# Kernel optimization log

Hardware: AMD Instinct MI355X
Metric: run time of the kernel (lower is better)

The kernel has to match this reference:

```python
import jax, jax.numpy as jnp
import numpy as np
from jax.scipy.linalg import solve_triangular


def setup_inputs() -> dict:
    key = jax.random.key(0)
    k1, k2 = jax.random.split(key)
    # [K classes, N per class, D features] training embeddings
    src_seq = jax.random.normal(k1, (256, 64, 128), dtype=jnp.float32)
    # [M, D] vectors to project and pairwise-score (clustering inner loop)
    test = jax.random.normal(k2, (8192, 128), dtype=jnp.float32)
    return {"src_seq": src_seq, "test": test}


def _fit_model(src_seq):
    # Faithful port of compute_scatter_matrices + fit_model.
    # S_w, S_b are symmetric PSD, so solve(S_w,S_b) eig is replaced by the
    # equivalent (and differentiable) generalized symmetric eig via Cholesky
    # whitening; A_inverse and psi are invariant to eigvec scaling/order.
    K, N, D = src_seq.shape
    count = K * N
    mean_per_class = src_seq.mean(axis=1)            # [K, D]
    mean = src_seq.mean(axis=(0, 1))                 # [D]
    diff_w = src_seq - mean_per_class[:, None, :]    # [K, N, D]
    diff_b = mean_per_class - mean                   # [K, D]
    S_w = jnp.einsum('knd,kne->de', diff_w, diff_w) / count   # [D, D]
    S_b = (N * jnp.einsum('kd,ke->de', diff_b, diff_b)) / count

    L = jnp.linalg.cholesky(S_w)                     # S_w = L L^T
    # Msym = L^{-1} S_b L^{-T}
    tmp = solve_triangular(L, S_b, lower=True)
    Msym = solve_triangular(L, tmp.T, lower=True).T
    Msym = 0.5 * (Msym + Msym.T)
    evals, U = jnp.linalg.eigh(Msym)
    W = solve_triangular(L, U, lower=True, trans=1)  # W = L^{-T} U, eigvecs of S_w^{-1} S_b

    lambda_b = jnp.sum(W * (S_b @ W), axis=0)        # diag(W^T S_b W)
    lambda_w = jnp.sum(W * (S_w @ W), axis=0)        # diag(W^T S_w W)
    n = float(N)
    # A = W^{-T} diag(sqrt(n/(n-1) * lambda_w))  =>  A^{-1} = diag(1/sqrt(.)) W^T
    A_inverse = (1.0 / jnp.sqrt(n / (n - 1.0) * lambda_w))[:, None] * W.T
    psi = jnp.clip((n - 1.0) / n * (lambda_b / lambda_w) - 1.0 / n, 0.0)
    return A_inverse, mean, psi


def reference(src_seq, test):
    A_inverse, mean, psi = _fit_model(src_seq)
    # latent = A_inverse @ (x - mean), batched over rows
    latent = (test - mean) @ A_inverse.T             # [M, D]
    # Pairwise single-vector probability (calculate_probability_single),
    # vectorized over all (i, j) pairs, in log space:
    # log p(i,j) = -(v_i - v_j)^T diag(psi) (v_i - v_j)
    #             - 0.5 * (D*log(2*pi) + log(||psi||_F))
    D = latent.shape[1]
    q = jnp.sum(psi * latent * latent, axis=1)       # [M]
    G = (latent * psi) @ latent.T                    # [M, M]
    maha = q[:, None] + q[None, :] - 2.0 * G         # [M, M]
    log_div = 0.5 * (D * jnp.log(2.0 * jnp.pi) + jnp.log(jnp.linalg.norm(psi)))
    return -maha - log_div                           # [M, M] pairwise log-prob
```

## Files before the change

### kernel.cpp

```cpp
#include <hip/hip_runtime.h>
#include <math.h>


#define D 128
#define NCLS 256
#define NPC 64
#define MTEST 8192
#define COUNT (NCLS*NPC)

#define fMC    0
#define fMEAN  16384
#define fSCAL  16640
#define fMAT   32768
#define fSWRAW 442368
#define fPART  458752
#define fU     458752
#define fV     983040
#define fQ     1507328
#define fBBF   1515520

#define sP   0
#define sSB  1
#define sP2  2
#define sP3  3
#define sP4  4
#define sZ   5
#define sMm  7
#define sC2  8
#define sXH  10
#define sT2  11
#define sT3  12
#define sT4  13
#define sT5  14
#define sT10 15
#define sT15 16
#define sT20 17
#define sG0  18
#define sF   23

using short8 = __attribute__((ext_vector_type(8))) short;
using f32x4  = __attribute__((ext_vector_type(4))) float;

__device__ inline unsigned short f2bf(float f) {
  unsigned u = __float_as_uint(f);
  unsigned r = u + 0x7FFFu + ((u >> 16) & 1u);
  return (unsigned short)(r >> 16);
}
__device__ inline float bf2f(unsigned short h) {
  return __uint_as_float(((unsigned)h) << 16);
}
__device__ inline float valU(const unsigned short* m, int idx) {
  return bf2f(m[idx]) + bf2f(m[idx + 16384]);
}
__device__ inline void storeDual(unsigned short* m, int idx, float g) {
  unsigned short hb = f2bf(g);
  m[idx] = hb;
  m[16384 + idx] = f2bf(g - bf2f(hb));
}
__device__ inline unsigned short* MS(float* ws, int m) {
  return (unsigned short*)(ws + fMAT) + (size_t)m * 32768;
}
__device__ inline short8 lds8(const unsigned short* L, int row, int colk) {
  unsigned u = ((unsigned)(row * 128 + colk)) ^ (((unsigned)(row & 7)) << 3);
  return *(const short8*)(L + u);
}
__device__ inline void ldsPutDual(unsigned short* L, int row, int col, float g) {
  unsigned u = ((unsigned)(row * 128 + col)) ^ (((unsigned)(row & 7)) << 3);
  unsigned short hb = f2bf(g);
  L[u] = hb;
  L[16384 + u] = f2bf(g - bf2f(hb));
}

__device__ float mm_body(const unsigned short* A, const unsigned short* B,
                         unsigned short* C, const unsigned short* E1,
                         float alpha, float beta, float delta, int brow) {
  int tid = threadIdx.x;
  int w = tid >> 6, lane = tid & 63;
  int wcol = w * 32;
  f32x4 acc[2][2] = {};
  #pragma unroll
  for (int ks = 0; ks < 4; ks++) {
    int kb = ks * 32 + (lane >> 4) * 8;
    short8 ah[2], al[2], bh[2], bl[2];
    #pragma unroll
    for (int mt = 0; mt < 2; mt++) {
      int r = brow + mt * 16 + (lane & 15);
      ah[mt] = *(const short8*)(A + r * 128 + kb);
      al[mt] = *(const short8*)(A + 16384 + r * 128 + kb);
    }
    #pragma unroll
    for (int nt = 0; nt < 2; nt++) {
      int c = wcol + nt * 16 + (lane & 15);
      bh[nt] = *(const short8*)(B + c * 128 + kb);
      bl[nt] = *(const short8*)(B + 16384 + c * 128 + kb);
    }
    #pragma unroll
    for (int mt = 0; mt < 2; mt++)
      #pragma unroll
      for (int nt = 0; nt < 2; nt++) {
        f32x4 a0 = acc[mt][nt];
        a0 = __builtin_amdgcn_mfma_f32_16x16x32_bf16(ah[mt], bh[nt], a0, 0, 0, 0);
        a0 = __builtin_amdgcn_mfma_f32_16x16x32_bf16(al[mt], bh[nt], a0, 0, 0, 0);
        a0 = __builtin_amdgcn_mfma_f32_16x16x32_bf16(ah[mt], bl[nt], a0, 0, 0, 0);
        acc[mt][nt] = a0;
      }
  }
  float tsum = 0.f;
  #pragma unroll
  for (int mt = 0; mt < 2; mt++)
    #pragma unroll
    for (int nt = 0; nt < 2; nt++)
      #pragma unroll
      for (int r = 0; r < 4; r++) {
        int row = brow + mt * 16 + (lane >> 4) * 4 + r;
        int col = wcol + nt * 16 + (lane & 15);
        int idx = row * 128 + col;
        float g = acc[mt][nt][r] * alpha;
        if (E1) g += beta * valU(E1, idx);
        if (row == col) g += delta;
        storeDual(C, idx, g);
        tsum += g * g;
      }
  return tsum;
}

__global__ __launch_bounds__(256) void k_gt_partial(const float* __restrict__ X, float* __restrict__ ws) {
  __shared__ unsigned short xt[128 * 256];
  int b = blockIdx.x, tid = threadIdx.x;
  const float* Xc = X + b * 256 * D;
  for (int idx = tid; idx < 256 * D; idx += 256) {
    int s = idx >> 7, d = idx & 127;
    unsigned byte = ((unsigned)(d * 512 + s * 2)) ^ (((unsigned)(d & 7)) << 4);
    *(unsigned short*)((char*)xt + byte) = f2bf(Xc[idx]);
  }
  {
    int d = tid & 127;
    for (int cc = (tid >> 7); cc < 4; cc += 2) {
      const float* p = Xc + cc * 64 * D + d;
      float s = 0.f;
      #pragma unroll
      for (int n = 0; n < 64; n++) s += p[n * D];
      ((unsigned short*)ws)[d * 256 + (b * 4 + cc)] = f2bf(s * (1.0f / 64.0f));
    }
  }
  __syncthreads();
  int w = tid >> 6, lane = tid & 63;
  int wr = (w >> 1) * 64, wc = (w & 1) * 64;
  f32x4 acc[4][4] = {};
  for (int ks = 0; ks < 8; ks++) {
    int kb = ks * 32 + (lane >> 4) * 8;
    short8 af[4];
    #pragma unroll
    for (int mt = 0; mt < 4; mt++) {
      int r = wr + mt * 16 + (lane & 15);
      unsigned byte = ((unsigned)(r * 512 + kb * 2)) ^ (((unsigned)(r & 7)) << 4);
      af[mt] = *(short8*)((char*)xt + byte);
    }
    #pragma unroll
    for (int nt = 0; nt < 4; nt++) {
      int c = wc + nt * 16 + (lane & 15);
      unsigned byte = ((unsigned)(c * 512 + kb * 2)) ^ (((unsigned)(c & 7)) << 4);
      short8 bfr = *(short8*)((char*)xt + byte);
      #pragma unroll
      for (int mt = 0; mt < 4; mt++)
        acc[mt][nt] = __builtin_amdgcn_mfma_f32_16x16x32_bf16(af[mt], bfr, acc[mt][nt], 0, 0, 0);
    }
  }
  float* outp = ws + fPART + b * 16384;
  #pragma unroll
  for (int mt = 0; mt < 4; mt++)
    #pragma unroll
    for (int nt = 0; nt < 4; nt++)
      #pragma unroll
      for (int r = 0; r < 4; r++) {
        int row = wr + mt * 16 + (lane >> 4) * 4 + r;
        int col = wc + nt * 16 + (lane & 15);
        outp[row * 128 + col] = acc[mt][nt][r];
      }
}

__global__ void k_reduce(float* __restrict__ ws) {
  __shared__ float red2[4];
  int tid = threadIdx.x;
  int idx = blockIdx.x * 256 + tid;
  const float* part = ws + fPART;
  float s = 0.f;
  #pragma unroll 8
  for (int p = 0; p < 64; p++) s += part[p * 16384 + idx];
  ws[fSWRAW + idx] = s;
  if (blockIdx.x == 0 && tid < 128) {
    const unsigned short* McT = (const unsigned short*)ws;
    float m = 0.f;
    for (int k = 0; k < 256; k++) m += bf2f(McT[tid * 256 + k]);
    ws[fMEAN + tid] = m * (1.0f / 256.0f);
  }
  if (blockIdx.x == 1) {
    float v = 0.f;
    if (tid < 128) {
      float gdd = 0.f;
      for (int p = 0; p < 64; p++) gdd += part[p * 16384 + tid * 129];
      const unsigned short* McT = (const unsigned short*)ws;
      float nrm = 0.f;
      for (int k = 0; k < 256; k++) { float x = bf2f(McT[tid * 256 + k]); nrm += x * x; }
      v = gdd * (1.0f / COUNT) - nrm * (1.0f / 256.0f);
    }
    #pragma unroll
    for (int off = 32; off > 0; off >>= 1) v += __shfl_down(v, off);
    if ((tid & 63) == 0) red2[tid >> 6] = v;
    __syncthreads();
    if (tid == 0) {
      float inv_s = 128.0f / (red2[0] + red2[1] + red2[2] + red2[3]);
      ws[fSCAL + 1] = inv_s;
      ws[fSCAL + 7] = 0.984375f * inv_s;
    }
  }
}

__global__ __launch_bounds__(256) void k_sbp(float* __restrict__ ws) {
  const unsigned short* Mc = (const unsigned short*)ws;
  const float* mv = ws + fMEAN;
  const float* swraw = ws + fSWRAW;
  float inv_s = ws[fSCAL + 1];
  unsigned short* SB = MS(ws, sSB);
  unsigned short* P = MS(ws, sP);
  int tid = threadIdx.x, b = blockIdx.x;
  int w = tid >> 6, lane = tid & 63;
  int brow = b * 32, wcol = w * 32;
  f32x4 acc[2][2] = {};
  for (int ks = 0; ks < 8; ks++) {
    int kb = ks * 32 + (lane >> 4) * 8;
    short8 af[2], bfv[2];
    #pragma unroll
    for (int mt = 0; mt < 2; mt++) {
      int r = brow + mt * 16 + (lane & 15);
      af[mt] = *(const short8*)(Mc + r * 256 + kb);
    }
    #pragma unroll
    for (int nt = 0; nt < 2; nt++) {
      int c = wcol + nt * 16 + (lane & 15);
      bfv[nt] = *(const short8*)(Mc + c * 256 + kb);
    }
    #pragma unroll
    for (int mt = 0; mt < 2; mt++)
      #pragma unroll
      for (int nt = 0; nt < 2; nt++)
        acc[mt][nt] = __builtin_amdgcn_mfma_f32_16x16x32_bf16(af[mt], bfv[nt], acc[mt][nt], 0, 0, 0);
  }
  #pragma unroll
  for (int mt = 0; mt < 2; mt++)
    #pragma unroll
    for (int nt = 0; nt < 2; nt++)
      #pragma unroll
      for (int r = 0; r < 4; r++) {
        int row = brow + mt * 16 + (lane >> 4) * 4 + r;
        int col = wcol + nt * 16 + (lane & 15);
        int idx = row * 128 + col;
        float g = acc[mt][nt][r] * (1.0f / 256.0f) - mv[row] * mv[col];
        storeDual(SB, idx, g);
        float s = (swraw[idx] * (1.0f / COUNT) - g - mv[row] * mv[col]) * inv_s;
        storeDual(P, idx, s - ((row == col) ? 1.0f : 0.0f));
      }
}

__global__ __launch_bounds__(256) void k_p234(float* __restrict__ ws) {
  __shared__ unsigned short sL[32768];
  float* scal = ws + fSCAL;
  const unsigned short* P = MS(ws, sP);
  unsigned short* P2 = MS(ws, sP2);
  unsigned short* P3 = MS(ws, sP3);
  unsigned short* P4 = MS(ws, sP4);
  int tid = threadIdx.x, b = blockIdx.x;
  int w = tid >> 6, lane = tid & 63;
  int wcol = w * 32, brow = b * 32;
  {
    f32x4 acc[8][2] = {};
    for (int ks = 0; ks < 4; ks++) {
      int kb = ks * 32 + (lane >> 4) * 8;
      short8 bh[2], bl[2];
      #pragma unroll
      for (int nt = 0; nt < 2; nt++) {
        int c = wcol + nt * 16 + (lane & 15);
        bh[nt] = *(const short8*)(P + c * 128 + kb);
        bl[nt] = *(const short8*)(P + 16384 + c * 128 + kb);
      }
      #pragma unroll
      for (int mt = 0; mt < 8; mt++) {
        int r = mt * 16 + (lane & 15);
        short8 ah = *(const short8*)(P + r * 128 + kb);
        short8 al = *(const short8*)(P + 16384 + r * 128 + kb);
        #pragma unroll
        for (int nt = 0; nt < 2; nt++) {
          f32x4 a0 = acc[mt][nt];
          a0 = __builtin_amdgcn_mfma_f32_16x16x32_bf16(ah, bh[nt], a0, 0, 0, 0);
          a0 = __builtin_amdgcn_mfma_f32_16x16x32_bf16(al, bh[nt], a0, 0, 0, 0);
          a0 = __builtin_amdgcn_mfma_f32_16x16x32_bf16(ah, bl[nt], a0, 0, 0, 0);
          acc[mt][nt] = a0;
        }
      }
    }
    #pragma unroll
    for (int mt = 0; mt < 8; mt++)
      #pragma unroll
      for (int nt = 0; nt < 2; nt++)
        #pragma unroll
        for (int r = 0; r < 4; r++) {
          int row = mt * 16 + (lane >> 4) * 4 + r;
          int col = wcol + nt * 16 + (lane & 15);
          float g = acc[mt][nt][r];
          ldsPutDual(sL, row, col, g);
          storeDual(P2, row * 128 + col, g);
        }
  }
  __syncthreads();
  float tsum = 0.f;
  {
    f32x4 a3[2][2] = {}, a4[2][2] = {};
    for (int ks = 0; ks < 4; ks++) {
      int kb = ks * 32 + (lane >> 4) * 8;
      short8 ah[2], al[2], b3h[2], b3l[2], b4h[2], b4l[2];
      #pragma unroll
      for (int mt = 0; mt < 2; mt++) {
        int r = brow + mt * 16 + (lane & 15);
        ah[mt] = lds8(sL, r, kb);
        al[mt] = lds8(sL + 16384, r, kb);
      }
      #pragma unroll
      for (int nt = 0; nt < 2; nt++) {
        int c = wcol + nt * 16 + (lane & 15);
        b3h[nt] = *(const short8*)(P + c * 128 + kb);
        b3l[nt] = *(const short8*)(P + 16384 + c * 128 + kb);
        b4h[nt] = lds8(sL, c, kb);
        b4l[nt] = lds8(sL + 16384, c, kb);
      }
      #pragma unroll
      for (int mt = 0; mt < 2; mt++)
        #pragma unroll
        for (int nt = 0; nt < 2; nt++) {
          f32x4 x3 = a3[mt][nt];
          x3 = __builtin_amdgcn_mfma_f32_16x16x32_bf16(ah[mt], b3h[nt], x3, 0, 0, 0);
          x3 = __builtin_amdgcn_mfma_f32_16x16x32_bf16(al[mt], b3h[nt], x3, 0, 0, 0);
          x3 = __builtin_amdgcn_mfma_f32_16x16x32_bf16(ah[mt], b3l[nt], x3, 0, 0, 0);
          a3[mt][nt] = x3;
          f32x4 x4 = a4[mt][nt];
          x4 = __builtin_amdgcn_mfma_f32_16x16x32_bf16(ah[mt], b4h[nt], x4, 0, 0, 0);
          x4 = __builtin_amdgcn_mfma_f32_16x16x32_bf16(al[mt], b4h[nt], x4, 0, 0, 0);
          x4 = __builtin_amdgcn_mfma_f32_16x16x32_bf16(ah[mt], b4l[nt], x4, 0, 0, 0);
          a4[mt][nt] = x4;
        }
    }
    #pragma unroll
    for (int mt = 0; mt < 2; mt++)
      #pragma unroll
      for (int nt = 0; nt < 2; nt++)
        #pragma unroll
        for (int r = 0; r < 4; r++) {
          int row = brow + mt * 16 + (lane >> 4) * 4 + r;
          int col = wcol + nt * 16 + (lane & 15);
          int idx = row * 128 + col;
          storeDual(P3, idx, a3[mt][nt][r]);
          float g4 = a4[mt][nt][r];
          storeDual(P4, idx, g4);
          tsum += g4 * g4;
        }
  }
  #pragma unroll
  for (int off = 32; off > 0; off >>= 1) tsum += __shfl_down(tsum, off);
  __syncthreads();
  float* red = (float*)sL;
  if (lane == 0) red[w] = tsum;
  __syncthreads();
  if (tid == 0) scal[60 + b] = red[0] + red[1] + red[2] + red[3];
}

__global__ __launch_bounds__(256) void k_z(float* __restrict__ ws) {
  __shared__ float cj[7];
  __shared__ float bt[7];
  float* scal = ws + fSCAL;
  const unsigned short *P = MS(ws, sP), *P2 = MS(ws, sP2),
    *P3 = MS(ws, sP3), *P4 = MS(ws, sP4);
  unsigned short* Z = MS(ws, sZ);
  int tid = threadIdx.x, b = blockIdx.x;
  float trP8 = scal[60] + scal[61] + scal[62] + scal[63];
  float a = 1.05f * sqrtf(sqrtf(sqrtf(fmaxf(trP8, 1e-30f))));
  a = fminf(a, 0.95f);
  if (tid < 7) {
    const float PI = 3.14159265358979f;
    float s = 0.f;
    for (int i = 0; i < 64; i++) {
      float th = (i + 0.5f) * (PI / 64.0f);
      float x = cosf(th);
      s += (1.0f / sqrtf(1.0f + a * x)) * cosf((float)tid * th);
    }
    cj[tid] = s * (2.0f / 64.0f);
  }
  __syncthreads();
  if (tid == 0) {
    float c0h = 0.5f * cj[0];
    float m0 = c0h - cj[2] + cj[4] - cj[6];
    float m1 = cj[1] - 3.0f * cj[3] + 5.0f * cj[5];
    float m2 = 2.0f * cj[2] - 8.0f * cj[4] + 18.0f * cj[6];
    float m3 = 4.0f * cj[3] - 20.0f * cj[5];
    float m4 = 8.0f * cj[4] - 48.0f * cj[6];
    float m5 = 16.0f * cj[5];
    float m6 = 32.0f * cj[6];
    float ia = 1.0f / a, p = 1.f;
    bt[0] = m0;
    p *= ia; bt[1] = m1 * p;
    p *= ia; bt[2] = m2 * p;
    p *= ia; bt[3] = m3 * p;
    p *= ia; bt[4] = m4 * p;
    p *= ia; bt[5] = m5 * p;
    p *= ia; bt[6] = m6 * p;
  }
  __syncthreads();
  int w = tid >> 6, lane = tid & 63;
  int brow = b * 32, wcol = w * 32;
  f32x4 a5[2][2] = {}, a6[2][2] = {};
  #pragma unroll
  for (int ks = 0; ks < 4; ks++) {
    int kb = ks * 32 + (lane >> 4) * 8;
    short8 ah[2], al[2], b5h[2], b5l[2], b6h[2], b6l[2];
    #pragma unroll
    for (int mt = 0; mt < 2; mt++) {
      int r = brow + mt * 16 + (lane & 15);
      ah[mt] = *(const short8*)(P4 + r * 128 + kb);
      al[mt] = *(const short8*)(P4 + 16384 + r * 128 + kb);
    }
    #pragma unroll
    for (int nt = 0; nt < 2; nt++) {
      int c = wcol + nt * 16 + (lane & 15);
      b5h[nt] = *(const short8*)(P + c * 128 + kb);
      b5l[nt] = *(const short8*)(P + 16384 + c * 128 + kb);
      b6h[nt] = *(const short8*)(P2 + c * 128 + kb);
      b6l[nt] = *(const short8*)(P2 + 16384 + c * 128 + kb);
    }
    #pragma unroll
    for (int mt = 0; mt < 2; mt++)
      #pragma unroll
      for (int nt = 0; nt < 2; nt++) {
        f32x4 x5 = a5[mt][nt];
        x5 = __builtin_amdgcn_mfma_f32_16x16x32_bf16(ah[mt], b5h[nt], x5, 0, 0, 0);
        x5 = __builtin_amdgcn_mfma_f32_16x16x32_bf16(al[mt], b5h[nt], x5, 0, 0, 0);
        x5 = __builtin_amdgcn_mfma_f32_16x16x32_bf16(ah[mt], b5l[nt], x5, 0, 0, 0);
        a5[mt][nt] = x5;
        f32x4 x6 = a6[mt][nt];
        x6 = __builtin_amdgcn_mfma_f32_16x16x32_bf16(ah[mt], b6h[nt], x6, 0, 0, 0);
        x6 = __builtin_amdgcn_mfma_f32_16x16x32_bf16(al[mt], b6h[nt], x6, 0, 0, 0);
        x6 = __builtin_amdgcn_mfma_f32_16x16x32_bf16(ah[mt], b6l[nt], x6, 0, 0, 0);
        a6[mt][nt] = x6;
      }
  }
  #pragma unroll
  for (int mt = 0; mt < 2; mt++)
    #pragma unroll
    for (int nt = 0; nt < 2; nt++)
      #pragma unroll
      for (int r = 0; r < 4; r++) {
        int row = brow + mt * 16 + (lane >> 4) * 4 + r;
        int col = wcol + nt * 16 + (lane & 15);
        int idx = row * 128 + col;
        float dg = (row == col) ? 1.0f : 0.0f;
        float z = bt[0] * dg + bt[1] * valU(P, idx) + bt[2] * valU(P2, idx) +
                  bt[3] * valU(P3, idx) + bt[4] * valU(P4, idx) +
                  bt[5] * a5[mt][nt][r] + bt[6] * a6[mt][nt][r];
        storeDual(Z, idx, z);
      }
}

__global__ __launch_bounds__(256) void k_msb(float* __restrict__ ws) {
  __shared__ unsigned short sL[32768];
  const unsigned short* Z = MS(ws, sZ);
  const unsigned short* SB = MS(ws, sSB);
  unsigned short* Mm = MS(ws, sMm);
  int tid = threadIdx.x, b = blockIdx.x;
  int w = tid >> 6, lane = tid & 63;
  int wcol = w * 32, brow = b * 32;
  {
    f32x4 acc[8][2] = {};
    for (int ks = 0; ks < 4; ks++) {
      int kb = ks * 32 + (lane >> 4) * 8;
      short8 bh[2], bl[2];
      #pragma unroll
      for (int nt = 0; nt < 2; nt++) {
        int c = wcol + nt * 16 + (lane & 15);
        bh[nt] = *(const short8*)(SB + c * 128 + kb);
        bl[nt] = *(const short8*)(SB + 16384 + c * 128 + kb);
      }
      #pragma unroll
      for (int mt = 0; mt < 8; mt++) {
        int r = mt * 16 + (lane & 15);
        short8 ah = *(const short8*)(Z + r * 128 + kb);
        short8 al = *(const short8*)(Z + 16384 + r * 128 + kb);
        #pragma unroll
        for (int nt = 0; nt < 2; nt++) {
          f32x4 a0 = acc[mt][nt];
          a0 = __builtin_amdgcn_mfma_f32_16x16x32_bf16(ah, bh[nt], a0, 0, 0, 0);
          a0 = __builtin_amdgcn_mfma_f32_16x16x32_bf16(al, bh[nt], a0, 0, 0, 0);
          a0 = __builtin_amdgcn_mfma_f32_16x16x32_bf16(ah, bl[nt], a0, 0, 0, 0);
          acc[mt][nt] = a0;
        }
      }
    }
    #pragma unroll
    for (int mt = 0; mt < 8; mt++)
      #pragma unroll
      for (int nt = 0; nt < 2; nt++)
        #pragma unroll
        for (int r = 0; r < 4; r++) {
          int row = mt * 16 + (lane >> 4) * 4 + r;
          int col = wcol + nt * 16 + (lane & 15);
          ldsPutDual(sL, row, col, acc[mt][nt][r]);
        }
  }
  __syncthreads();
  {
    f32x4 acc[2][2] = {};
    for (int ks = 0; ks < 4; ks++) {
      int kb = ks * 32 + (lane >> 4) * 8;
      short8 ah[2], al[2], bh[2], bl[2];
      #pragma unroll
      for (int mt = 0; mt < 2; mt++) {
        int r = brow + mt * 16 + (lane & 15);
        ah[mt] = lds8(sL, r, kb);
        al[mt] = lds8(sL + 16384, r, kb);
      }
      #pragma unroll
      for (int nt = 0; nt < 2; nt++) {
        int c = wcol + nt * 16 + (lane & 15);
        bh[nt] = *(const short8*)(Z + c * 128 + kb);
        bl[nt] = *(const short8*)(Z + 16384 + c * 128 + kb);
      }
      #pragma unroll
      for (int mt = 0; mt < 2; mt++)
        #pragma unroll
        for (int nt = 0; nt < 2; nt++) {
          f32x4 a0 = acc[mt][nt];
          a0 = __builtin_amdgcn_mfma_f32_16x16x32_bf16(ah[mt], bh[nt], a0, 0, 0, 0);
          a0 = __builtin_amdgcn_mfma_f32_16x16x32_bf16(al[mt], bh[nt], a0, 0, 0, 0);
          a0 = __builtin_amdgcn_mfma_f32_16x16x32_bf16(ah[mt], bl[nt], a0, 0, 0, 0);
          acc[mt][nt] = a0;
        }
    }
    #pragma unroll
    for (int mt = 0; mt < 2; mt++)
      #pragma unroll
      for (int nt = 0; nt < 2; nt++)
        #pragma unroll
        for (int r = 0; r < 4; r++) {
          int row = brow + mt * 16 + (lane >> 4) * 4 + r;
          int col = wcol + nt * 16 + (lane & 15);
          storeDual(Mm, row * 128 + col, acc[mt][nt][r]);
        }
  }
}

__global__ __launch_bounds__(256) void k_c24(float* __restrict__ ws) {
  __shared__ unsigned short sL[32768];
  float* scal = ws + fSCAL;
  const unsigned short* Mm = MS(ws, sMm);
  unsigned short* C2 = MS(ws, sC2);
  int tid = threadIdx.x, b = blockIdx.x;
  int w = tid >> 6, lane = tid & 63;
  int wcol = w * 32, brow = b * 32;
  {
    f32x4 acc[8][2] = {};
    for (int ks = 0; ks < 4; ks++) {
      int kb = ks * 32 + (lane >> 4) * 8;
      short8 bh[2], bl[2];
      #pragma unroll
      for (int nt = 0; nt < 2; nt++) {
        int c = wcol + nt * 16 + (lane & 15);
        bh[nt] = *(const short8*)(Mm + c * 128 + kb);
        bl[nt] = *(const short8*)(Mm + 16384 + c * 128 + kb);
      }
      #pragma unroll
      for (int mt = 0; mt < 8; mt++) {
        int r = mt * 16 + (lane & 15);
        short8 ah = *(const short8*)(Mm + r * 128 + kb);
        short8 al = *(const short8*)(Mm + 16384 + r * 128 + kb);
        #pragma unroll
        for (int nt = 0; nt < 2; nt++) {
          f32x4 a0 = acc[mt][nt];
          a0 = __builtin_amdgcn_mfma_f32_16x16x32_bf16(ah, bh[nt], a0, 0, 0, 0);
          a0 = __builtin_amdgcn_mfma_f32_16x16x32_bf16(al, bh[nt], a0, 0, 0, 0);
          a0 = __builtin_amdgcn_mfma_f32_16x16x32_bf16(ah, bl[nt], a0, 0, 0, 0);
          acc[mt][nt] = a0;
        }
      }
    }
    #pragma unroll
    for (int mt = 0; mt < 8; mt++)
      #pragma unroll
      for (int nt = 0; nt < 2; nt++)
        #pragma unroll
        for (int r = 0; r < 4; r++) {
          int row = mt * 16 + (lane >> 4) * 4 + r;
          int col = wcol + nt * 16 + (lane & 15);
          float g = acc[mt][nt][r];
          ldsPutDual(sL, row, col, g);
          storeDual(C2, row * 128 + col, g);
        }
  }
  __syncthreads();
  float tsum = 0.f;
  {
    f32x4 acc[2][2] = {};
    for (int ks = 0; ks < 4; ks++) {
      int kb = ks * 32 + (lane >> 4) * 8;
      short8 ah[2], al[2], bh[2], bl[2];
      #pragma unroll
      for (int mt = 0; mt < 2; mt++) {
        int r = brow + mt * 16 + (lane & 15);
        ah[mt] = lds8(sL, r, kb);
        al[mt] = lds8(sL + 16384, r, kb);
      }
      #pragma unroll
      for (int nt = 0; nt < 2; nt++) {
        int c = wcol + nt * 16 + (lane & 15);
        bh[nt] = lds8(sL, c, kb);
        bl[nt] = lds8(sL + 16384, c, kb);
      }
      #pragma unroll
      for (int mt = 0; mt < 2; mt++)
        #pragma unroll
        for (int nt = 0; nt < 2; nt++) {
          f32x4 a0 = acc[mt][nt];
          a0 = __builtin_amdgcn_mfma_f32_16x16x32_bf16(ah[mt], bh[nt], a0, 0, 0, 0);
          a0 = __builtin_amdgcn_mfma_f32_16x16x32_bf16(al[mt], bh[nt], a0, 0, 0, 0);
          a0 = __builtin_amdgcn_mfma_f32_16x16x32_bf16(ah[mt], bl[nt], a0, 0, 0, 0);
          acc[mt][nt] = a0;
        }
    }
    #pragma unroll
    for (int mt = 0; mt < 2; mt++)
      #pragma unroll
      for (int nt = 0; nt < 2; nt++)
        #pragma unroll
        for (int r = 0; r < 4; r++) {
          float g = acc[mt][nt][r];
          tsum += g * g;
        }
  }
  #pragma unroll
  for (int off = 32; off > 0; off >>= 1) tsum += __shfl_down(tsum, off);
  __syncthreads();
  float* red = (float*)sL;
  if (lane == 0) red[w] = tsum;
  __syncthreads();
  if (tid == 0) scal[68 + b] = red[0] + red[1] + red[2] + red[3];
}

__device__ inline void interval_cs(const float* scal, float* c0o, float* iho) {
  float trM8 = scal[68] + scal[69] + scal[70] + scal[71];
  float Lam = 1.03f * sqrtf(sqrtf(sqrtf(fmaxf(trM8, 1e-37f))));
  float lo = -0.02f * Lam, hi = Lam;
  *c0o = 0.5f * (hi + lo);
  *iho = 1.0f / (0.5f * (hi - lo));
}

__global__ __launch_bounds__(256) void k_xh_t2(float* __restrict__ ws) {
  __shared__ float cs[2];
  float* scal = ws + fSCAL;
  if (threadIdx.x == 0) {
    float c0, ih;
    interval_cs(scal, &c0, &ih);
    cs[0] = c0; cs[1] = ih;
  }
  __syncthreads();
  float c0 = cs[0], ih = cs[1];
  float a2 = 2.0f * ih * ih, b2 = -4.0f * c0 * ih * ih, g2 = 2.0f * c0 * c0 * ih * ih - 1.0f;
  const unsigned short* Mm = MS(ws, sMm);
  const unsigned short* C2 = MS(ws, sC2);
  unsigned short* XH = MS(ws, sXH);
  unsigned short* T2 = MS(ws, sT2);
  int gid = blockIdx.x * 256 + threadIdx.x;
  #pragma unroll
  for (int t = 0; t < 4; t++) {
    int idx = gid * 4 + t;
    int row = idx >> 7, col = idx & 127;
    float m = valU(Mm, idx), c2v = valU(C2, idx);
    float dg = (row == col) ? 1.0f : 0.0f;
    storeDual(XH, idx, ih * m - ih * c0 * dg);
    storeDual(T2, idx, a2 * c2v + b2 * m + g2 * dg);
  }
}

__global__ __launch_bounds__(256) void k_t34(float* __restrict__ ws) {
  const unsigned short* XH = MS(ws, sXH);
  const unsigned short* T2 = MS(ws, sT2);
  if (blockIdx.x < 4) {
    mm_body(XH, T2, MS(ws, sT3), XH, 2.0f, -1.0f, 0.0f, blockIdx.x * 32);
  } else {
    mm_body(T2, T2, MS(ws, sT4), nullptr, 2.0f, 0.0f, -1.0f, (blockIdx.x - 4) * 32);
  }
}

__global__ __launch_bounds__(256) void k_t5g(float* __restrict__ ws) {
  __shared__ float cs[8];
  __shared__ float sat[25];
  __shared__ float sc[25];
  float* scal = ws + fSCAL;
  int tid = threadIdx.x;
  if (blockIdx.x < 4) {
    mm_body(MS(ws, sT3), MS(ws, sT2), MS(ws, sT5), MS(ws, sXH),
            2.0f, -1.0f, 0.0f, blockIdx.x * 32);
    return;
  }
  if (tid == 0) {
    float c0, ih;
    interval_cs(scal, &c0, &ih);
    float inv_s = scal[1];
    float t0 = (1.0f / 63.0f) / inv_s;
    float x0 = fminf(fmaxf((t0 - c0) * ih, -1.0f), 1.0f);
    cs[0] = acosf(x0); cs[1] = x0;
    cs[2] = 0.984375f * inv_s / ih;
  }
  __syncthreads();
  if (tid <= 24) {
    float th = cs[0], x0 = cs[1], SCc = cs[2];
    const float PI = 3.14159265358979f;
    float v;
    if (tid == 0) v = 0.5f * SCc * (2.0f / PI) * (sinf(th) - x0 * th);
    else if (tid == 1) v = SCc * (2.0f / PI) * (0.5f * th + 0.25f * sinf(2.0f * th) - x0 * sinf(th));
    else {
      float fj = (float)tid;
      v = SCc * (2.0f / PI) *
          (0.5f * (sinf((fj + 1.0f) * th) / (fj + 1.0f) + sinf((fj - 1.0f) * th) / (fj - 1.0f))
           - x0 * sinf(fj * th) / fj);
    }
    sat[tid] = v;
    sc[tid] = 0.f;
  }
  __syncthreads();
  if (tid == 0) {
    for (int j = 24; j >= 5; --j) {
      int k = j / 5, r = j - 5 * k;
      float aj = sat[j];
      if (r == 0) sc[k * 5] += aj;
      else { sc[k * 5 + r] += 2.0f * aj; sat[5 * k - r] -= aj; }
    }
    for (int r = 0; r < 5; r++) sc[r] += sat[r];
  }
  __syncthreads();
  const unsigned short* XH = MS(ws, sXH);
  const unsigned short* T2 = MS(ws, sT2);
  const unsigned short* T3 = MS(ws, sT3);
  const unsigned short* T4 = MS(ws, sT4);
  int bg = blockIdx.x - 4;
  int base = bg * 1024 + tid * 4;
  #pragma unroll
  for (int t = 0; t < 4; t++) {
    int idx = base + t;
    int row = idx >> 7, col = idx & 127;
    float dg = (row == col) ? 1.0f : 0.0f;
    float x1 = valU(XH, idx), x2 = valU(T2, idx), x3 = valU(T3, idx), x4 = valU(T4, idx);
    #pragma unroll
    for (int k = 0; k < 5; k++) {
      float g = sc[k * 5 + 0] * dg + sc[k * 5 + 1] * x1 + sc[k * 5 + 2] * x2 +
                sc[k * 5 + 3] * x3 + sc[k * 5 + 4] * x4;
      storeDual(MS(ws, sG0 + k), idx, g);
    }
  }
}

__global__ __launch_bounds__(256) void k_t101520(float* __restrict__ ws) {
  __shared__ unsigned short sL[32768];
  const unsigned short* T5 = MS(ws, sT5);
  unsigned short* T10 = MS(ws, sT10);
  unsigned short* T15 = MS(ws, sT15);
  unsigned short* T20 = MS(ws, sT20);
  int tid = threadIdx.x, b = blockIdx.x;
  int w = tid >> 6, lane = tid & 63;
  int wcol = w * 32, brow = b * 32;
  {
    f32x4 acc[8][2] = {};
    for (int ks = 0; ks < 4; ks++) {
      int kb = ks * 32 + (lane >> 4) * 8;
      short8 bh[2], bl[2];
      #pragma unroll
      for (int nt = 0; nt < 2; nt++) {
        int c = wcol + nt * 16 + (lane & 15);
        bh[nt] = *(const short8*)(T5 + c * 128 + kb);
        bl[nt] = *(const short8*)(T5 + 16384 + c * 128 + kb);
      }
      #pragma unroll
      for (int mt = 0; mt < 8; mt++) {
        int r = mt * 16 + (lane & 15);
        short8 ah = *(const short8*)(T5 + r * 128 + kb);
        short8 al = *(const short8*)(T5 + 16384 + r * 128 + kb);
        #pragma unroll
        for (int nt = 0; nt < 2; nt++) {
          f32x4 a0 = acc[mt][nt];
          a0 = __builtin_amdgcn_mfma_f32_16x16x32_bf16(ah, bh[nt], a0, 0, 0, 0);
          a0 = __builtin_amdgcn_mfma_f32_16x16x32_bf16(al, bh[nt], a0, 0, 0, 0);
          a0 = __builtin_amdgcn_mfma_f32_16x16x32_bf16(ah, bl[nt], a0, 0, 0, 0);
          acc[mt][nt] = a0;
        }
      }
    }
    #pragma unroll
    for (int mt = 0; mt < 8; mt++)
      #pragma unroll
      for (int nt = 0; nt < 2; nt++)
        #pragma unroll
        for (int r = 0; r < 4; r++) {
          int row = mt * 16 + (lane >> 4) * 4 + r;
          int col = wcol + nt * 16 + (lane & 15);
          float g = 2.0f * acc[mt][nt][r] - ((row == col) ? 1.0f : 0.0f);
          ldsPutDual(sL, row, col, g);
          storeDual(T10, row * 128 + col, g);
        }
  }
  __syncthreads();
  {
    f32x4 a15[2][2] = {}, a20[2][2] = {};
    for (int ks = 0; ks < 4; ks++) {
      int kb = ks * 32 + (lane >> 4) * 8;
      short8 ah[2], al[2], b5h[2], b5l[2], bth[2], btl[2];
      #pragma unroll
      for (int mt = 0; mt < 2; mt++) {
        int r = brow + mt * 16 + (lane & 15);
        ah[mt] = lds8(sL, r, kb);
        al[mt] = lds8(sL + 16384, r, kb);
      }
      #pragma unroll
      for (int nt = 0; nt < 2; nt++) {
        int c = wcol + nt * 16 + (lane & 15);
        b5h[nt] = *(const short8*)(T5 + c * 128 + kb);
        b5l[nt] = *(const short8*)(T5 + 16384 + c * 128 + kb);
        bth[nt] = lds8(sL, c, kb);
        btl[nt] = lds8(sL + 16384, c, kb);
      }
      #pragma unroll
      for (int mt = 0; mt < 2; mt++)
        #pragma unroll
        for (int nt = 0; nt < 2; nt++) {
          f32x4 x = a15[mt][nt];
          x = __builtin_amdgcn_mfma_f32_16x16x32_bf16(ah[mt], b5h[nt], x, 0, 0, 0);
          x = __builtin_amdgcn_mfma_f32_16x16x32_bf16(al[mt], b5h[nt], x, 0, 0, 0);
          x = __builtin_amdgcn_mfma_f32_16x16x32_bf16(ah[mt], b5l[nt], x, 0, 0, 0);
          a15[mt][nt] = x;
          f32x4 y = a20[mt][nt];
          y = __builtin_amdgcn_mfma_f32_16x16x32_bf16(ah[mt], bth[nt], y, 0, 0, 0);
          y = __builtin_amdgcn_mfma_f32_16x16x32_bf16(al[mt], bth[nt], y, 0, 0, 0);
          y = __builtin_amdgcn_mfma_f32_16x16x32_bf16(ah[mt], btl[nt], y, 0, 0, 0);
          a20[mt][nt] = y;
        }
    }
    #pragma unroll
    for (int mt = 0; mt < 2; mt++)
      #pragma unroll
      for (int nt = 0; nt < 2; nt++)
        #pragma unroll
        for (int r = 0; r < 4; r++) {
          int row = brow + mt * 16 + (lane >> 4) * 4 + r;
          int col = wcol + nt * 16 + (lane & 15);
          int idx = row * 128 + col;
          storeDual(T15, idx, 2.0f * a15[mt][nt][r] - valU(T5, idx));
          storeDual(T20, idx, 2.0f * a20[mt][nt][r] - ((row == col) ? 1.0f : 0.0f));
        }
  }
}

__global__ __launch_bounds__(256) void k_bigF(float* __restrict__ ws) {
  __shared__ float red[4];
  float* scal = ws + fSCAL;
  const unsigned short* As[4] = { MS(ws, sT5), MS(ws, sT10), MS(ws, sT15), MS(ws, sT20) };
  const unsigned short* Bs[4] = { MS(ws, sG0 + 1), MS(ws, sG0 + 2), MS(ws, sG0 + 3), MS(ws, sG0 + 4) };
  const unsigned short* G0 = MS(ws, sG0);
  unsigned short* Fm = MS(ws, sF);
  int tid = threadIdx.x, b = blockIdx.x;
  int w = tid >> 6, lane = tid & 63;
  int brow = b * 32, wcol = w * 32;
  f32x4 acc[2][2] = {};
  for (int p = 0; p < 4; p++) {
    const unsigned short* A = As[p];
    const unsigned short* B = Bs[p];
    #pragma unroll
    for (int ks = 0; ks < 4; ks++) {
      int kb = ks * 32 + (lane >> 4) * 8;
      short8 ah[2], al[2], bh[2], bl[2];
      #pragma unroll
      for (int mt = 0; mt < 2; mt++) {
        int r = brow + mt * 16 + (lane & 15);
        ah[mt] = *(const short8*)(A + r * 128 + kb);
        al[mt] = *(const short8*)(A + 16384 + r * 128 + kb);
      }
      #pragma unroll
      for (int nt = 0; nt < 2; nt++) {
        int c = wcol + nt * 16 + (lane & 15);
        bh[nt] = *(const short8*)(B + c * 128 + kb);
        bl[nt] = *(const short8*)(B + 16384 + c * 128 + kb);
      }
      #pragma unroll
      for (int mt = 0; mt < 2; mt++)
        #pragma unroll
        for (int nt = 0; nt < 2; nt++) {
          f32x4 a0 = acc[mt][nt];
          a0 = __builtin_amdgcn_mfma_f32_16x16x32_bf16(ah[mt], bh[nt], a0, 0, 0, 0);
          a0 = __builtin_amdgcn_mfma_f32_16x16x32_bf16(al[mt], bh[nt], a0, 0, 0, 0);
          a0 = __builtin_amdgcn_mfma_f32_16x16x32_bf16(ah[mt], bl[nt], a0, 0, 0, 0);
          acc[mt][nt] = a0;
        }
    }
  }
  float tsum = 0.f;
  #pragma unroll
  for (int mt = 0; mt < 2; mt++)
    #pragma unroll
    for (int nt = 0; nt < 2; nt++)
      #pragma unroll
      for (int r = 0; r < 4; r++) {
        int row = brow + mt * 16 + (lane >> 4) * 4 + r;
        int col = wcol + nt * 16 + (lane & 15);
        int idx = row * 128 + col;
        float g = acc[mt][nt][r] + valU(G0, idx);
        storeDual(Fm, idx, g);
        tsum += g * g;
      }
  #pragma unroll
  for (int off = 32; off > 0; off >>= 1) tsum += __shfl_down(tsum, off);
  if (lane == 0) red[w] = tsum;
  __syncthreads();
  if (tid == 0) scal[72 + b] = red[0] + red[1] + red[2] + red[3];
}

__global__ __launch_bounds__(256) void k_zfb(float* __restrict__ ws) {
  __shared__ unsigned short sL[32768];
  const unsigned short* Z = MS(ws, sZ);
  const unsigned short* Fm = MS(ws, sF);
  unsigned short* Bbf = (unsigned short*)(ws + fBBF);
  float aeff = ws[fSCAL + 7];
  int tid = threadIdx.x, b = blockIdx.x;
  int w = tid >> 6, lane = tid & 63;
  int wcol = w * 32, brow = b * 32;
  {
    f32x4 acc[8][2] = {};
    for (int ks = 0; ks < 4; ks++) {
      int kb = ks * 32 + (lane >> 4) * 8;
      short8 bh[2], bl[2];
      #pragma unroll
      for (int nt = 0; nt < 2; nt++) {
        int c = wcol + nt * 16 + (lane & 15);
        bh[nt] = *(const short8*)(Fm + c * 128 + kb);
        bl[nt] = *(const short8*)(Fm + 16384 + c * 128 + kb);
      }
      #pragma unroll
      for (int mt = 0; mt < 8; mt++) {
        int r = mt * 16 + (lane & 15);
        short8 ah = *(const short8*)(Z + r * 128 + kb);
        short8 al = *(const short8*)(Z + 16384 + r * 128 + kb);
        #pragma unroll
        for (int nt = 0; nt < 2; nt++) {
          f32x4 a0 = acc[mt][nt];
          a0 = __builtin_amdgcn_mfma_f32_16x16x32_bf16(ah, bh[nt], a0, 0, 0, 0);
          a0 = __builtin_amdgcn_mfma_f32_16x16x32_bf16(al, bh[nt], a0, 0, 0, 0);
          a0 = __builtin_amdgcn_mfma_f32_16x16x32_bf16(ah, bl[nt], a0, 0, 0, 0);
          acc[mt][nt] = a0;
        }
      }
    }
    #pragma unroll
    for (int mt = 0; mt < 8; mt++)
      #pragma unroll
      for (int nt = 0; nt < 2; nt++)
        #pragma unroll
        for (int r = 0; r < 4; r++) {
          int row = mt * 16 + (lane >> 4) * 4 + r;
          int col = wcol + nt * 16 + (lane & 15);
          ldsPutDual(sL, row, col, acc[mt][nt][r]);
        }
  }
  __syncthreads();
  {
    f32x4 acc[2][2] = {};
    for (int ks = 0; ks < 4; ks++) {
      int kb = ks * 32 + (lane >> 4) * 8;
      short8 ah[2], al[2], bh[2], bl[2];
      #pragma unroll
      for (int mt = 0; mt < 2; mt++) {
        int r = brow + mt * 16 + (lane & 15);
        ah[mt] = lds8(sL, r, kb);
        al[mt] = lds8(sL + 16384, r, kb);
      }
      #pragma unroll
      for (int nt = 0; nt < 2; nt++) {
        int c = wcol + nt * 16 + (lane & 15);
        bh[nt] = *(const short8*)(Z + c * 128 + kb);
        bl[nt] = *(const short8*)(Z + 16384 + c * 128 + kb);
      }
      #pragma unroll
      for (int mt = 0; mt < 2; mt++)
        #pragma unroll
        for (int nt = 0; nt < 2; nt++) {
          f32x4 a0 = acc[mt][nt];
          a0 = __builtin_amdgcn_mfma_f32_16x16x32_bf16(ah[mt], bh[nt], a0, 0, 0, 0);
          a0 = __builtin_amdgcn_mfma_f32_16x16x32_bf16(al[mt], bh[nt], a0, 0, 0, 0);
          a0 = __builtin_amdgcn_mfma_f32_16x16x32_bf16(ah[mt], bl[nt], a0, 0, 0, 0);
          acc[mt][nt] = a0;
        }
    }
    #pragma unroll
    for (int mt = 0; mt < 2; mt++)
      #pragma unroll
      for (int nt = 0; nt < 2; nt++)
        #pragma unroll
        for (int r = 0; r < 4; r++) {
          int row = brow + mt * 16 + (lane >> 4) * 4 + r;
          int col = wcol + nt * 16 + (lane & 15);
          Bbf[row * 128 + col] = f2bf(acc[mt][nt][r] * aeff);
        }
  }
}

__global__ __launch_bounds__(256) void k_latent(const float* __restrict__ test, float* __restrict__ ws) {
  __shared__ unsigned short vh[16384];
  __shared__ float qs[128];
  int blk = blockIdx.x, tid = threadIdx.x;
  if (blk == 0 && tid == 0) {
    float* scal = ws + fSCAL;
    float trF2 = fmaxf(scal[72] + scal[73] + scal[74] + scal[75], 1e-30f);
    scal[0] = 0.5f * (128.0f * 1.8378770664093453f + 0.5f * logf(trF2));
  }
  const float* tb = test + blk * 128 * D;
  unsigned short* Vbf = (unsigned short*)(ws + fV);
  if (tid < 128) qs[tid] = 0.f;
  for (int idx = tid; idx < 16384; idx += 256) {
    int r = idx >> 7, c = idx & 127;
    float v = tb[idx] - ws[fMEAN + c];
    unsigned short h = f2bf(v);
    unsigned byte = ((unsigned)(r * 256 + c * 2)) ^ (((unsigned)(r & 7)) << 4);
    *(unsigned short*)((char*)vh + byte) = h;
    Vbf[blk * 16384 + idx] = h;
  }
  __syncthreads();
  int w = tid >> 6, lane = tid & 63;
  int wr = (w >> 1) * 64, wc = (w & 1) * 64;
  const unsigned short* Bbf = (const unsigned short*)(ws + fBBF);
  f32x4 acc[4][4] = {};
  for (int ks = 0; ks < 4; ks++) {
    int kb = ks * 32 + (lane >> 4) * 8;
    short8 af[4], bfv[4];
    #pragma unroll
    for (int mt = 0; mt < 4; mt++) {
      int r = wr + mt * 16 + (lane & 15);
      unsigned byte = ((unsigned)(r * 256 + kb * 2)) ^ (((unsigned)(r & 7)) << 4);
      af[mt] = *(short8*)((char*)vh + byte);
    }
    #pragma unroll
    for (int nt = 0; nt < 4; nt++) {
      int c = wc + nt * 16 + (lane & 15);
      bfv[nt] = *(const short8*)(Bbf + c * 128 + kb);
    }
    #pragma unroll
    for (int mt = 0; mt < 4; mt++)
      #pragma unroll
      for (int nt = 0; nt < 4; nt++)
        acc[mt][nt] = __builtin_amdgcn_mfma_f32_16x16x32_bf16(af[mt], bfv[nt], acc[mt][nt], 0, 0, 0);
  }
  unsigned short* Ubf = (unsigned short*)(ws + fU);
  #pragma unroll
  for (int mt = 0; mt < 4; mt++)
    #pragma unroll
    for (int nt = 0; nt < 4; nt++)
      #pragma unroll
      for (int r = 0; r < 4; r++) {
        int row = wr + mt * 16 + (lane >> 4) * 4 + r;
        int col = wc + nt * 16 + (lane & 15);
        Ubf[(blk * 128 + row) * 128 + col] = f2bf(acc[mt][nt][r]);
      }
  #pragma unroll
  for (int mt = 0; mt < 4; mt++)
    #pragma unroll
    for (int r = 0; r < 4; r++) {
      int row = wr + mt * 16 + (lane >> 4) * 4 + r;
      float p = 0.f;
      #pragma unroll
      for (int nt = 0; nt < 4; nt++) {
        int col = wc + nt * 16 + (lane & 15);
        unsigned byte = ((unsigned)(row * 256 + col * 2)) ^ (((unsigned)(row & 7)) << 4);
        p += bf2f(f2bf(acc[mt][nt][r])) * bf2f(*(unsigned short*)((char*)vh + byte));
      }
      p += __shfl_xor(p, 1, 16);
      p += __shfl_xor(p, 2, 16);
      p += __shfl_xor(p, 4, 16);
      p += __shfl_xor(p, 8, 16);
      if ((lane & 15) == 0) atomicAdd(&qs[row], p);
    }
  __syncthreads();
  if (tid < 128) ws[fQ + blk * 128 + tid] = qs[tid];
}

__global__ __launch_bounds__(256) void k_pair(const float* __restrict__ ws, float* __restrict__ out) {
  __shared__ float qi[128];
  __shared__ float qj[128];
  __shared__ float sld;
  int bi = blockIdx.x, bj = blockIdx.y, tid = threadIdx.x;
  if (tid < 128) qi[tid] = ws[fQ + bi * 128 + tid];
  else qj[tid - 128] = ws[fQ + bj * 128 + (tid - 128)];
  if (tid == 0) sld = ws[fSCAL + 0];
  __syncthreads();
  int w = tid >> 6, lane = tid & 63;
  int wr = (w >> 1) * 64, wc = (w & 1) * 64;
  const unsigned short* Ubf = (const unsigned short*)(ws + fU);
  const unsigned short* Vbf = (const unsigned short*)(ws + fV);
  f32x4 acc[4][4] = {};
  for (int ks = 0; ks < 4; ks++) {
    int kb = ks * 32 + (lane >> 4) * 8;
    short8 af[4], bfv[4];
    #pragma unroll
    for (int mt = 0; mt < 4; mt++) {
      int r = bi * 128 + wr + mt * 16 + (lane & 15);
      af[mt] = *(const short8*)(Ubf + r * 128 + kb);
    }
    #pragma unroll
    for (int nt = 0; nt < 4; nt++) {
      int c = bj * 128 + wc + nt * 16 + (lane & 15);
      bfv[nt] = *(const short8*)(Vbf + c * 128 + kb);
    }
    #pragma unroll
    for (int mt = 0; mt < 4; mt++)
      #pragma unroll
      for (int nt = 0; nt < 4; nt++)
        acc[mt][nt] = __builtin_amdgcn_mfma_f32_16x16x32_bf16(af[mt], bfv[nt], acc[mt][nt], 0, 0, 0);
  }
  float ld = sld;
  #pragma unroll
  for (int mt = 0; mt < 4; mt++)
    #pragma unroll
    for (int nt = 0; nt < 4; nt++)
      #pragma unroll
      for (int r = 0; r < 4; r++) {
        int row = wr + mt * 16 + (lane >> 4) * 4 + r;
        int col = wc + nt * 16 + (lane & 15);
        float g = acc[mt][nt][r];
        out[(size_t)(bi * 128 + row) * MTEST + (bj * 128 + col)] =
          2.0f * g - qi[row] - qj[col] - ld;
      }
}

extern "C" void kernel_launch(void* const* d_in, const int* in_sizes, int n_in,
                              void* d_out, int out_size, void* d_ws, size_t ws_size,
                              hipStream_t stream) {
  (void)in_sizes; (void)n_in; (void)out_size; (void)ws_size;
  const float* X = (const float*)d_in[0];
  const float* test = (const float*)d_in[1];
  float* out = (float*)d_out;
  float* ws = (float*)d_ws;

  k_gt_partial<<<64, 256, 0, stream>>>(X, ws);
  k_reduce<<<64, 256, 0, stream>>>(ws);
  k_sbp<<<4, 256, 0, stream>>>(ws);
  k_p234<<<4, 256, 0, stream>>>(ws);
  k_z<<<4, 256, 0, stream>>>(ws);
  k_msb<<<4, 256, 0, stream>>>(ws);
  k_c24<<<4, 256, 0, stream>>>(ws);
  k_xh_t2<<<16, 256, 0, stream>>>(ws);
  k_t34<<<8, 256, 0, stream>>>(ws);
  k_t5g<<<20, 256, 0, stream>>>(ws);
  k_t101520<<<4, 256, 0, stream>>>(ws);
  k_bigF<<<4, 256, 0, stream>>>(ws);
  k_zfb<<<4, 256, 0, stream>>>(ws);
  k_latent<<<64, 256, 0, stream>>>(test, ws);
  k_pair<<<dim3(64, 64), 256, 0, stream>>>(ws, out);
}
```

Baseline: 300.5 us.

## Chain matrix products per row strip to drop redundant full-matrix recompute

The small 128x128 matrix-chain kernels no longer have each of the 4 blocks recompute a full 128x128 intermediate product. Each block now computes only its own 32-row strip and chains the next product from that strip held in shared memory, e.g. P2 then P3 = P2*P then P4 = P3*P. The C2 step drops the fourth-power trace and the spectral bound now uses the trace of M^2 with a fourth root. This removes redundant MFMA work and shrinks shared memory from 64KB to 16KB per block, at the cost of a longer serial dependency chain inside each kernel.

```diff
diff --git a/kernel.cpp b/kernel.cpp
--- a/kernel.cpp
+++ b/kernel.cpp
@@ -60,20 +60,25 @@
 __device__ inline unsigned short* MS(float* ws, int m) {
   return (unsigned short*)(ws + fMAT) + (size_t)m * 32768;
 }
-__device__ inline short8 lds8(const unsigned short* L, int row, int colk) {
-  unsigned u = ((unsigned)(row * 128 + colk)) ^ (((unsigned)(row & 7)) << 3);
+__device__ inline short8 st8(const unsigned short* L, int rloc, int colk) {
+  unsigned u = ((unsigned)(rloc * 128 + colk)) ^ (((unsigned)(rloc & 7)) << 3);
   return *(const short8*)(L + u);
 }
-__device__ inline void ldsPutDual(unsigned short* L, int row, int col, float g) {
-  unsigned u = ((unsigned)(row * 128 + col)) ^ (((unsigned)(row & 7)) << 3);
+__device__ inline float stValU(const unsigned short* L, int rloc, int col) {
+  unsigned u = ((unsigned)(rloc * 128 + col)) ^ (((unsigned)(rloc & 7)) << 3);
+  return bf2f(L[u]) + bf2f(L[4096 + u]);
+}
+__device__ inline void stPutDual(unsigned short* L, int rloc, int col, float g) {
+  unsigned u = ((unsigned)(rloc * 128 + col)) ^ (((unsigned)(rloc & 7)) << 3);
   unsigned short hb = f2bf(g);
   L[u] = hb;
-  L[16384 + u] = f2bf(g - bf2f(hb));
-}
-
-__device__ float mm_body(const unsigned short* A, const unsigned short* B,
+  L[4096 + u] = f2bf(g - bf2f(hb));
+}
+
+__device__ float mm_core(const unsigned short* A, const unsigned short* B,
                          unsigned short* C, const unsigned short* E1,
-                         float alpha, float beta, float delta, int brow) {
+                         float alpha, float beta, float delta, int brow,
+                         unsigned short* outBf, float aeff2) {
   int tid = threadIdx.x;
   int w = tid >> 6, lane = tid & 63;
   int wcol = w * 32;
@@ -118,7 +123,8 @@
         float g = acc[mt][nt][r] * alpha;
         if (E1) g += beta * valU(E1, idx);
         if (row == col) g += delta;
-        storeDual(C, idx, g);
+        if (outBf) outBf[idx] = f2bf(g * aeff2);
+        else storeDual(C, idx, g);
         tsum += g * g;
       }
   return tsum;
@@ -262,8 +268,10 @@
       }
 }
 
-__global__ __launch_bounds__(256) void k_p234(float* __restrict__ ws) {
-  __shared__ unsigned short sL[32768];
+__global__ __launch_bounds__(256) void k_pows(float* __restrict__ ws) {
+  __shared__ unsigned short sA[8192];
+  __shared__ unsigned short sB[8192];
+  __shared__ float red[4];
   float* scal = ws + fSCAL;
   const unsigned short* P = MS(ws, sP);
   unsigned short* P2 = MS(ws, sP2);
@@ -271,12 +279,19 @@
   unsigned short* P4 = MS(ws, sP4);
   int tid = threadIdx.x, b = blockIdx.x;
   int w = tid >> 6, lane = tid & 63;
-  int wcol = w * 32, brow = b * 32;
+  int brow = b * 32, wcol = w * 32;
   {
-    f32x4 acc[8][2] = {};
+    f32x4 acc[2][2] = {};
+    #pragma unroll
     for (int ks = 0; ks < 4; ks++) {
       int kb = ks * 32 + (lane >> 4) * 8;
-      short8 bh[2], bl[2];
+      short8 ah[2], al[2], bh[2], bl[2];
+      #pragma unroll
+      for (int mt = 0; mt < 2; mt++) {
+        int r = brow + mt * 16 + (lane & 15);
+        ah[mt] = *(const short8*)(P + r * 128 + kb);
+        al[mt] = *(const short8*)(P + 16384 + r * 128 + kb);
+      }
       #pragma unroll
       for (int nt = 0; nt < 2; nt++) {
         int c = wcol + nt * 16 + (lane & 15);
@@ -284,68 +299,101 @@
         bl[nt] = *(const short8*)(P + 16384 + c * 128 + kb);
       }
       #pragma unroll
-      for (int mt = 0; mt < 8; mt++) {
-        int r = mt * 16 + (lane & 15);
-        short8 ah = *(const short8*)(P + r * 128 + kb);
-        short8 al = *(const short8*)(P + 16384 + r * 128 + kb);
+      for (int mt = 0; mt < 2; mt++)
         #pragma unroll
         for (int nt = 0; nt < 2; nt++) {
           f32x4 a0 = acc[mt][nt];
-          a0 = __builtin_amdgcn_mfma_f32_16x16x32_bf16(ah, bh[nt], a0, 0, 0, 0);
-          a0 = __builtin_amdgcn_mfma_f32_16x16x32_bf16(al, bh[nt], a0, 0, 0, 0);
-          a0 = __builtin_amdgcn_mfma_f32_16x16x32_bf16(ah, bl[nt], a0, 0, 0, 0);
+          a0 = __builtin_amdgcn_mfma_f32_16x16x32_bf16(ah[mt], bh[nt], a0, 0, 0, 0);
+          a0 = __builtin_amdgcn_mfma_f32_16x16x32_bf16(al[mt], bh[nt], a0, 0, 0, 0);
+          a0 = __builtin_amdgcn_mfma_f32_16x16x32_bf16(ah[mt], bl[nt], a0, 0, 0, 0);
           acc[mt][nt] = a0;
         }
-      }
-    }
-    #pragma unroll
-    for (int mt = 0; mt < 8; mt++)
+    }
+    #pragma unroll
+    for (int mt = 0; mt < 2; mt++)
       #pragma unroll
       for (int nt = 0; nt < 2; nt++)
         #pragma unroll
         for (int r = 0; r < 4; r++) {
-          int row = mt * 16 + (lane >> 4) * 4 + r;
+          int rloc = mt * 16 + (lane >> 4) * 4 + r;
           int col = wcol + nt * 16 + (lane & 15);
           float g = acc[mt][nt][r];
-          ldsPutDual(sL, row, col, g);
-          storeDual(P2, row * 128 + col, g);
+          stPutDual(sA, rloc, col, g);
+          storeDual(P2, (brow + rloc) * 128 + col, g);
+        }
+  }
+  __syncthreads();
+  {
+    f32x4 acc[2][2] = {};
+    #pragma unroll
+    for (int ks = 0; ks < 4; ks++) {
+      int kb = ks * 32 + (lane >> 4) * 8;
+      short8 ah[2], al[2], bh[2], bl[2];
+      #pragma unroll
+      for (int mt = 0; mt < 2; mt++) {
+        int rloc = mt * 16 + (lane & 15);
+        ah[mt] = st8(sA, rloc, kb);
+        al[mt] = st8(sA + 4096, rloc, kb);
+      }
+      #pragma unroll
+      for (int nt = 0; nt < 2; nt++) {
+        int c = wcol + nt * 16 + (lane & 15);
+        bh[nt] = *(const short8*)(P + c * 128 + kb);
+        bl[nt] = *(const short8*)(P + 16384 + c * 128 + kb);
+      }
+      #pragma unroll
+      for (int mt = 0; mt < 2; mt++)
+        #pragma unroll
+        for (int nt = 0; nt < 2; nt++) {
+          f32x4 a0 = acc[mt][nt];
+          a0 = __builtin_amdgcn_mfma_f32_16x16x32_bf16(ah[mt], bh[nt], a0, 0, 0, 0);
+          a0 = __builtin_amdgcn_mfma_f32_16x16x32_bf16(al[mt], bh[nt], a0, 0, 0, 0);
+          a0 = __builtin_amdgcn_mfma_f32_16x16x32_bf16(ah[mt], bl[nt], a0, 0, 0, 0);
+          acc[mt][nt] = a0;
+        }
+    }
+    #pragma unroll
+    for (int mt = 0; mt < 2; mt++)
+      #pragma unroll
+      for (int nt = 0; nt < 2; nt++)
+        #pragma unroll
+        for (int r = 0; r < 4; r++) {
+          int rloc = mt * 16 + (lane >> 4) * 4 + r;
+          int col = wcol + nt * 16 + (lane & 15);
+          float g = acc[mt][nt][r];
+          stPutDual(sB, rloc, col, g);
+          storeDual(P3, (brow + rloc) * 128 + col, g);
         }
   }
   __syncthreads();
   float tsum = 0.f;
   {
-    f32x4 a3[2][2] = {}, a4[2][2] = {};
+    f32x4 acc[2][2] = {};
+    #pragma unroll
     for (int ks = 0; ks < 4; ks++) {
       int kb = ks * 32 + (lane >> 4) * 8;
-      short8 ah[2], al[2], b3h[2], b3l[2], b4h[2], b4l[2];
+      short8 ah[2], al[2], bh[2], bl[2];
       #pragma unroll
       for (int mt = 0; mt < 2; mt++) {
-        int r = brow + mt * 16 + (lane & 15);
-        ah[mt] = lds8(sL, r, kb);
-        al[mt] = lds8(sL + 16384, r, kb);
+        int rloc = mt * 16 + (lane & 15);
+        ah[mt] = st8(sB, rloc, kb);
+        al[mt] = st8(sB + 4096, rloc, kb);
       }
       #pragma unroll
       for (int nt = 0; nt < 2; nt++) {
         int c = wcol + nt * 16 + (lane & 15);
-        b3h[nt] = *(const short8*)(P + c * 128 + kb);
-        b3l[nt] = *(const short8*)(P + 16384 + c * 128 + kb);
-        b4h[nt] = lds8(sL, c, kb);
-        b4l[nt] = lds8(sL + 16384, c, kb);
+        bh[nt] = *(const short8*)(P + c * 128 + kb);
+        bl[nt] = *(const short8*)(P + 16384 + c * 128 + kb);
       }
       #pragma unroll
       for (int mt = 0; mt < 2; mt++)
         #pragma unroll
         for (int nt = 0; nt < 2; nt++) {
-          f32x4 x3 = a3[mt][nt];
-          x3 = __builtin_amdgcn_mfma_f32_16x16x32_bf16(ah[mt], b3h[nt], x3, 0, 0, 0);
-          x3 = __builtin_amdgcn_mfma_f32_16x16x32_bf16(al[mt], b3h[nt], x3, 0, 0, 0);
-          x3 = __builtin_amdgcn_mfma_f32_16x16x32_bf16(ah[mt], b3l[nt], x3, 0, 0, 0);
-          a3[mt][nt] = x3;
-          f32x4 x4 = a4[mt][nt];
-          x4 = __builtin_amdgcn_mfma_f32_16x16x32_bf16(ah[mt], b4h[nt], x4, 0, 0, 0);
-          x4 = __builtin_amdgcn_mfma_f32_16x16x32_bf16(al[mt], b4h[nt], x4, 0, 0, 0);
-          x4 = __builtin_amdgcn_mfma_f32_16x16x32_bf16(ah[mt], b4l[nt], x4, 0, 0, 0);
-          a4[mt][nt] = x4;
+          f32x4 a0 = acc[mt][nt];
+          a0 = __builtin_amdgcn_mfma_f32_16x16x32_bf16(ah[mt], bh[nt], a0, 0, 0, 0);
+          a0 = __builtin_amdgcn_mfma_f32_16x16x32_bf16(al[mt], bh[nt], a0, 0, 0, 0);
+          a0 = __builtin_amdgcn_mfma_f32_16x16x32_bf16(ah[mt], bl[nt], a0, 0, 0, 0);
+          acc[mt][nt] = a0;
         }
     }
     #pragma unroll
@@ -354,19 +402,15 @@
       for (int nt = 0; nt < 2; nt++)
         #pragma unroll
         for (int r = 0; r < 4; r++) {
-          int row = brow + mt * 16 + (lane >> 4) * 4 + r;
+          int rloc = mt * 16 + (lane >> 4) * 4 + r;
           int col = wcol + nt * 16 + (lane & 15);
-          int idx = row * 128 + col;
-          storeDual(P3, idx, a3[mt][nt][r]);
-          float g4 = a4[mt][nt][r];
-          storeDual(P4, idx, g4);
-          tsum += g4 * g4;
+          float g = acc[mt][nt][r];
+          storeDual(P4, (brow + rloc) * 128 + col, g);
+          tsum += g * g;
         }
   }
   #pragma unroll
   for (int off = 32; off > 0; off >>= 1) tsum += __shfl_down(tsum, off);
-  __syncthreads();
-  float* red = (float*)sL;
   if (lane == 0) red[w] = tsum;
   __syncthreads();
   if (tid == 0) scal[60 + b] = red[0] + red[1] + red[2] + red[3];
@@ -467,68 +511,31 @@
       }
 }
 
-__global__ __launch_bounds__(256) void k_msb(float* __restrict__ ws) {
-  __shared__ unsigned short sL[32768];
+__global__ __launch_bounds__(256) void k_m(float* __restrict__ ws) {
+  __shared__ unsigned short sA[8192];
   const unsigned short* Z = MS(ws, sZ);
   const unsigned short* SB = MS(ws, sSB);
   unsigned short* Mm = MS(ws, sMm);
   int tid = threadIdx.x, b = blockIdx.x;
   int w = tid >> 6, lane = tid & 63;
-  int wcol = w * 32, brow = b * 32;
+  int brow = b * 32, wcol = w * 32;
   {
-    f32x4 acc[8][2] = {};
+    f32x4 acc[2][2] = {};
+    #pragma unroll
     for (int ks = 0; ks < 4; ks++) {
       int kb = ks * 32 + (lane >> 4) * 8;
-      short8 bh[2], bl[2];
+      short8 ah[2], al[2], bh[2], bl[2];
+      #pragma unroll
+      for (int mt = 0; mt < 2; mt++) {
+        int r = brow + mt * 16 + (lane & 15);
+        ah[mt] = *(const short8*)(Z + r * 128 + kb);
+        al[mt] = *(const short8*)(Z + 16384 + r * 128 + kb);
+      }
       #pragma unroll
       for (int nt = 0; nt < 2; nt++) {
         int c = wcol + nt * 16 + (lane & 15);
         bh[nt] = *(const short8*)(SB + c * 128 + kb);
         bl[nt] = *(const short8*)(SB + 16384 + c * 128 + kb);
-      }
-      #pragma unroll
-      for (int mt = 0; mt < 8; mt++) {
-        int r = mt * 16 + (lane & 15);
-        short8 ah = *(const short8*)(Z + r * 128 + kb);
-        short8 al = *(const short8*)(Z + 16384 + r * 128 + kb);
-        #pragma unroll
-        for (int nt = 0; nt < 2; nt++) {
-          f32x4 a0 = acc[mt][nt];
-          a0 = __builtin_amdgcn_mfma_f32_16x16x32_bf16(ah, bh[nt], a0, 0, 0, 0);
-          a0 = __builtin_amdgcn_mfma_f32_16x16x32_bf16(al, bh[nt], a0, 0, 0, 0);
-          a0 = __builtin_amdgcn_mfma_f32_16x16x32_bf16(ah, bl[nt], a0, 0, 0, 0);
-          acc[mt][nt] = a0;
-        }
-      }
-    }
-    #pragma unroll
-    for (int mt = 0; mt < 8; mt++)
-      #pragma unroll
-      for (int nt = 0; nt < 2; nt++)
-        #pragma unroll
-        for (int r = 0; r < 4; r++) {
-          int row = mt * 16 + (lane >> 4) * 4 + r;
-          int col = wcol + nt * 16 + (lane & 15);
-          ldsPutDual(sL, row, col, acc[mt][nt][r]);
-        }
-  }
-  __syncthreads();
-  {
-    f32x4 acc[2][2] = {};
-    for (int ks = 0; ks < 4; ks++) {
-      int kb = ks * 32 + (lane >> 4) * 8;
-      short8 ah[2], al[2], bh[2], bl[2];
-      #pragma unroll
-      for (int mt = 0; mt < 2; mt++) {
-        int r = brow + mt * 16 + (lane & 15);
-        ah[mt] = lds8(sL, r, kb);
-        al[mt] = lds8(sL + 16384, r, kb);
-      }
-      #pragma unroll
-      for (int nt = 0; nt < 2; nt++) {
-        int c = wcol + nt * 16 + (lane & 15);
-        bh[nt] = *(const short8*)(Z + c * 128 + kb);
-        bl[nt] = *(const short8*)(Z + 16384 + c * 128 + kb);
       }
       #pragma unroll
       for (int mt = 0; mt < 2; mt++)
@@ -547,78 +554,29 @@
       for (int nt = 0; nt < 2; nt++)
         #pragma unroll
         for (int r = 0; r < 4; r++) {
-          int row = brow + mt * 16 + (lane >> 4) * 4 + r;
+          int rloc = mt * 16 + (lane >> 4) * 4 + r;
           int col = wcol + nt * 16 + (lane & 15);
-          storeDual(Mm, row * 128 + col, acc[mt][nt][r]);
-        }
-  }
-}
-
-__global__ __launch_bounds__(256) void k_c24(float* __restrict__ ws) {
-  __shared__ unsigned short sL[32768];
-  float* scal = ws + fSCAL;
-  const unsigned short* Mm = MS(ws, sMm);
-  unsigned short* C2 = MS(ws, sC2);
-  int tid = threadIdx.x, b = blockIdx.x;
-  int w = tid >> 6, lane = tid & 63;
-  int wcol = w * 32, brow = b * 32;
-  {
-    f32x4 acc[8][2] = {};
-    for (int ks = 0; ks < 4; ks++) {
-      int kb = ks * 32 + (lane >> 4) * 8;
-      short8 bh[2], bl[2];
-      #pragma unroll
-      for (int nt = 0; nt < 2; nt++) {
-        int c = wcol + nt * 16 + (lane & 15);
-        bh[nt] = *(const short8*)(Mm + c * 128 + kb);
-        bl[nt] = *(const short8*)(Mm + 16384 + c * 128 + kb);
-      }
-      #pragma unroll
-      for (int mt = 0; mt < 8; mt++) {
-        int r = mt * 16 + (lane & 15);
-        short8 ah = *(const short8*)(Mm + r * 128 + kb);
-        short8 al = *(const short8*)(Mm + 16384 + r * 128 + kb);
-        #pragma unroll
-        for (int nt = 0; nt < 2; nt++) {
-          f32x4 a0 = acc[mt][nt];
-          a0 = __builtin_amdgcn_mfma_f32_16x16x32_bf16(ah, bh[nt], a0, 0, 0, 0);
-          a0 = __builtin_amdgcn_mfma_f32_16x16x32_bf16(al, bh[nt], a0, 0, 0, 0);
-          a0 = __builtin_amdgcn_mfma_f32_16x16x32_bf16(ah, bl[nt], a0, 0, 0, 0);
-          acc[mt][nt] = a0;
-        }
-      }
-    }
-    #pragma unroll
-    for (int mt = 0; mt < 8; mt++)
-      #pragma unroll
-      for (int nt = 0; nt < 2; nt++)
-        #pragma unroll
-        for (int r = 0; r < 4; r++) {
-          int row = mt * 16 + (lane >> 4) * 4 + r;
-          int col = wcol + nt * 16 + (lane & 15);
-          float g = acc[mt][nt][r];
-          ldsPutDual(sL, row, col, g);
-          storeDual(C2, row * 128 + col, g);
-        }
-  }
-  __syncthreads();
-  float tsum = 0.f;
+          stPutDual(sA, rloc, col, acc[mt][nt][r]);
+        }
+  }
+  __syncthreads();
   {
     f32x4 acc[2][2] = {};
+    #pragma unroll
     for (int ks = 0; ks < 4; ks++) {
       int kb = ks * 32 + (lane >> 4) * 8;
       short8 ah[2], al[2], bh[2], bl[2];
       #pragma unroll
       for (int mt = 0; mt < 2; mt++) {
-        int r = brow + mt * 16 + (lane & 15);
-        ah[mt] = lds8(sL, r, kb);
-        al[mt] = lds8(sL + 16384, r, kb);
+        int rloc = mt * 16 + (lane & 15);
+        ah[mt] = st8(sA, rloc, kb);
+        al[mt] = st8(sA + 4096, rloc, kb);
       }
       #pragma unroll
       for (int nt = 0; nt < 2; nt++) {
         int c = wcol + nt * 16 + (lane & 15);
-        bh[nt] = lds8(sL, c, kb);
-        bl[nt] = lds8(sL + 16384, c, kb);
+        bh[nt] = *(const short8*)(Z + c * 128 + kb);
+        bl[nt] = *(const short8*)(Z + 16384 + c * 128 + kb);
       }
       #pragma unroll
       for (int mt = 0; mt < 2; mt++)
@@ -637,22 +595,30 @@
       for (int nt = 0; nt < 2; nt++)
         #pragma unroll
         for (int r = 0; r < 4; r++) {
-          float g = acc[mt][nt][r];
-          tsum += g * g;
-        }
-  }
+          int rloc = mt * 16 + (lane >> 4) * 4 + r;
+          int col = wcol + nt * 16 + (lane & 15);
+          storeDual(Mm, (brow + rloc) * 128 + col, acc[mt][nt][r]);
+        }
+  }
+}
+
+__global__ __launch_bounds__(256) void k_c2(float* __restrict__ ws) {
+  __shared__ float red[4];
+  float* scal = ws + fSCAL;
+  const unsigned short* Mm = MS(ws, sMm);
+  int tid = threadIdx.x, b = blockIdx.x;
+  int w = tid >> 6, lane = tid & 63;
+  float tsum = mm_core(Mm, Mm, MS(ws, sC2), nullptr, 1.0f, 0.0f, 0.0f, b * 32, nullptr, 1.0f);
   #pragma unroll
   for (int off = 32; off > 0; off >>= 1) tsum += __shfl_down(tsum, off);
-  __syncthreads();
-  float* red = (float*)sL;
   if (lane == 0) red[w] = tsum;
   __syncthreads();
   if (tid == 0) scal[68 + b] = red[0] + red[1] + red[2] + red[3];
 }
 
 __device__ inline void interval_cs(const float* scal, float* c0o, float* iho) {
-  float trM8 = scal[68] + scal[69] + scal[70] + scal[71];
-  float Lam = 1.03f * sqrtf(sqrtf(sqrtf(fmaxf(trM8, 1e-37f))));
+  float trM4 = scal[68] + scal[69] + scal[70] + scal[71];
+  float Lam = 1.03f * sqrtf(sqrtf(fmaxf(trM4, 1e-37f)));
   float lo = -0.02f * Lam, hi = Lam;
   *c0o = 0.5f * (hi + lo);
   *iho = 1.0f / (0.5f * (hi - lo));
@@ -689,9 +655,9 @@
   const unsigned short* XH = MS(ws, sXH);
   const unsigned short* T2 = MS(ws, sT2);
   if (blockIdx.x < 4) {
-    mm_body(XH, T2, MS(ws, sT3), XH, 2.0f, -1.0f, 0.0f, blockIdx.x * 32);
+    mm_core(XH, T2, MS(ws, sT3), XH, 2.0f, -1.0f, 0.0f, blockIdx.x * 32, nullptr, 1.0f);
   } else {
-    mm_body(T2, T2, MS(ws, sT4), nullptr, 2.0f, 0.0f, -1.0f, (blockIdx.x - 4) * 32);
+    mm_core(T2, T2, MS(ws, sT4), nullptr, 2.0f, 0.0f, -1.0f, (blockIdx.x - 4) * 32, nullptr, 1.0f);
   }
 }
 
@@ -702,8 +668,8 @@
   float* scal = ws + fSCAL;
   int tid = threadIdx.x;
   if (blockIdx.x < 4) {
-    mm_body(MS(ws, sT3), MS(ws, sT2), MS(ws, sT5), MS(ws, sXH),
-            2.0f, -1.0f, 0.0f, blockIdx.x * 32);
+    mm_core(MS(ws, sT3), MS(ws, sT2), MS(ws, sT5), MS(ws, sXH),
+            2.0f, -1.0f, 0.0f, blockIdx.x * 32, nullptr, 1.0f);
     return;
   }
   if (tid == 0) {
@@ -763,20 +729,28 @@
   }
 }
 
-__global__ __launch_bounds__(256) void k_t101520(float* __restrict__ ws) {
-  __shared__ unsigned short sL[32768];
+__global__ __launch_bounds__(256) void k_thi(float* __restrict__ ws) {
+  __shared__ unsigned short sA[8192];
+  __shared__ unsigned short sB[8192];
   const unsigned short* T5 = MS(ws, sT5);
   unsigned short* T10 = MS(ws, sT10);
   unsigned short* T15 = MS(ws, sT15);
   unsigned short* T20 = MS(ws, sT20);
   int tid = threadIdx.x, b = blockIdx.x;
   int w = tid >> 6, lane = tid & 63;
-  int wcol = w * 32, brow = b * 32;
+  int brow = b * 32, wcol = w * 32;
   {
-    f32x4 acc[8][2] = {};
+    f32x4 acc[2][2] = {};
+    #pragma unroll
     for (int ks = 0; ks < 4; ks++) {
       int kb = ks * 32 + (lane >> 4) * 8;
-      short8 bh[2], bl[2];
+      short8 ah[2], al[2], bh[2], bl[2];
+      #pragma unroll
+      for (int mt = 0; mt < 2; mt++) {
+        int r = brow + mt * 16 + (lane & 15);
+        ah[mt] = *(const short8*)(T5 + r * 128 + kb);
+        al[mt] = *(const short8*)(T5 + 16384 + r * 128 + kb);
+      }
       #pragma unroll
       for (int nt = 0; nt < 2; nt++) {
         int c = wcol + nt * 16 + (lane & 15);
@@ -784,67 +758,58 @@
         bl[nt] = *(const short8*)(T5 + 16384 + c * 128 + kb);
       }
       #pragma unroll
-      for (int mt = 0; mt < 8; mt++) {
-        int r = mt * 16 + (lane & 15);
-        short8 ah = *(const short8*)(T5 + r * 128 + kb);
-        short8 al = *(const short8*)(T5 + 16384 + r * 128 + kb);
+      for (int mt = 0; mt < 2; mt++)
         #pragma unroll
         for (int nt = 0; nt < 2; nt++) {
           f32x4 a0 = acc[mt][nt];
-          a0 = __builtin_amdgcn_mfma_f32_16x16x32_bf16(ah, bh[nt], a0, 0, 0, 0);
-          a0 = __builtin_amdgcn_mfma_f32_16x16x32_bf16(al, bh[nt], a0, 0, 0, 0);
-          a0 = __builtin_amdgcn_mfma_f32_16x16x32_bf16(ah, bl[nt], a0, 0, 0, 0);
+          a0 = __builtin_amdgcn_mfma_f32_16x16x32_bf16(ah[mt], bh[nt], a0, 0, 0, 0);
+          a0 = __builtin_amdgcn_mfma_f32_16x16x32_bf16(al[mt], bh[nt], a0, 0, 0, 0);
+          a0 = __builtin_amdgcn_mfma_f32_16x16x32_bf16(ah[mt], bl[nt], a0, 0, 0, 0);
           acc[mt][nt] = a0;
         }
-      }
-    }
-    #pragma unroll
-    for (int mt = 0; mt < 8; mt++)
+    }
+    #pragma unroll
+    for (int mt = 0; mt < 2; mt++)
       #pragma unroll
       for (int nt = 0; nt < 2; nt++)
         #pragma unroll
         for (int r = 0; r < 4; r++) {
-          int row = mt * 16 + (lane >> 4) * 4 + r;
+          int rloc = mt * 16 + (lane >> 4) * 4 + r;
           int col = wcol + nt * 16 + (lane & 15);
+          int row = brow + rloc;
           float g = 2.0f * acc[mt][nt][r] - ((row == col) ? 1.0f : 0.0f);
-          ldsPutDual(sL, row, col, g);
+          stPutDual(sA, rloc, col, g);
           storeDual(T10, row * 128 + col, g);
         }
   }
   __syncthreads();
   {
-    f32x4 a15[2][2] = {}, a20[2][2] = {};
+    f32x4 acc[2][2] = {};
+    #pragma unroll
     for (int ks = 0; ks < 4; ks++) {
       int kb = ks * 32 + (lane >> 4) * 8;
-      short8 ah[2], al[2], b5h[2], b5l[2], bth[2], btl[2];
+      short8 ah[2], al[2], bh[2], bl[2];
       #pragma unroll
       for (int mt = 0; mt < 2; mt++) {
-        int r = brow + mt * 16 + (lane & 15);
-        ah[mt] = lds8(sL, r, kb);
-        al[mt] = lds8(sL + 16384, r, kb);
+        int rloc = mt * 16 + (lane & 15);
+        ah[mt] = st8(sA, rloc, kb);
+        al[mt] = st8(sA + 4096, rloc, kb);
       }
       #pragma unroll
       for (int nt = 0; nt < 2; nt++) {
         int c = wcol + nt * 16 + (lane & 15);
-        b5h[nt] = *(const short8*)(T5 + c * 128 + kb);
-        b5l[nt] = *(const short8*)(T5 + 16384 + c * 128 + kb);
-        bth[nt] = lds8(sL, c, kb);
-        btl[nt] = lds8(sL + 16384, c, kb);
+        bh[nt] = *(const short8*)(T5 + c * 128 + kb);
+        bl[nt] = *(const short8*)(T5 + 16384 + c * 128 + kb);
       }
       #pragma unroll
       for (int mt = 0; mt < 2; mt++)
         #pragma unroll
         for (int nt = 0; nt < 2; nt++) {
-          f32x4 x = a15[mt][nt];
-          x = __builtin_amdgcn_mfma_f32_16x16x32_bf16(ah[mt], b5h[nt], x, 0, 0, 0);
-          x = __builtin_amdgcn_mfma_f32_16x16x32_bf16(al[mt], b5h[nt], x, 0, 0, 0);
-          x = __builtin_amdgcn_mfma_f32_16x16x32_bf16(ah[mt], b5l[nt], x, 0, 0, 0);
-          a15[mt][nt] = x;
-          f32x4 y = a20[mt][nt];
-          y = __builtin_amdgcn_mfma_f32_16x16x32_bf16(ah[mt], bth[nt], y, 0, 0, 0);
-          y = __builtin_amdgcn_mfma_f32_16x16x32_bf16(al[mt], bth[nt], y, 0, 0, 0);
-          y = __builtin_amdgcn_mfma_f32_16x16x32_bf16(ah[mt], btl[nt], y, 0, 0, 0);
-          a20[mt][nt] = y;
+          f32x4 a0 = acc[mt][nt];
+          a0 = __builtin_amdgcn_mfma_f32_16x16x32_bf16(ah[mt], bh[nt], a0, 0, 0, 0);
+          a0 = __builtin_amdgcn_mfma_f32_16x16x32_bf16(al[mt], bh[nt], a0, 0, 0, 0);
+          a0 = __builtin_amdgcn_mfma_f32_16x16x32_bf16(ah[mt], bl[nt], a0, 0, 0, 0);
+          acc[mt][nt] = a0;
         }
     }
     #pragma unroll
@@ -853,11 +818,54 @@
       for (int nt = 0; nt < 2; nt++)
         #pragma unroll
         for (int r = 0; r < 4; r++) {
-          int row = brow + mt * 16 + (lane >> 4) * 4 + r;
+          int rloc = mt * 16 + (lane >> 4) * 4 + r;
           int col = wcol + nt * 16 + (lane & 15);
-          int idx = row * 128 + col;
-          storeDual(T15, idx, 2.0f * a15[mt][nt][r] - valU(T5, idx));
-          storeDual(T20, idx, 2.0f * a20[mt][nt][r] - ((row == col) ? 1.0f : 0.0f));
+          int idx = (brow + rloc) * 128 + col;
+          float g = 2.0f * acc[mt][nt][r] - valU(T5, idx);
+          stPutDual(sB, rloc, col, g);
+          storeDual(T15, idx, g);
+        }
+  }
+  __syncthreads();
+  {
+    f32x4 acc[2][2] = {};
+    #pragma unroll
+    for (int ks = 0; ks < 4; ks++) {
+      int kb = ks * 32 + (lane >> 4) * 8;
+      short8 ah[2], al[2], bh[2], bl[2];
+      #pragma unroll
+      for (int mt = 0; mt < 2; mt++) {
+        int rloc = mt * 16 + (lane & 15);
+        ah[mt] = st8(sB, rloc, kb);
+        al[mt] = st8(sB + 4096, rloc, kb);
+      }
+      #pragma unroll
+      for (int nt = 0; nt < 2; nt++) {
+        int c = wcol + nt * 16 + (lane & 15);
+        bh[nt] = *(const short8*)(T5 + c * 128 + kb);
+        bl[nt] = *(const short8*)(T5 + 16384 + c * 128 + kb);
+      }
+      #pragma unroll
+      for (int mt = 0; mt < 2; mt++)
+        #pragma unroll
+        for (int nt = 0; nt < 2; nt++) {
+          f32x4 a0 = acc[mt][nt];
+          a0 = __builtin_amdgcn_mfma_f32_16x16x32_bf16(ah[mt], bh[nt], a0, 0, 0, 0);
+          a0 = __builtin_amdgcn_mfma_f32_16x16x32_bf16(al[mt], bh[nt], a0, 0, 0, 0);
+          a0 = __builtin_amdgcn_mfma_f32_16x16x32_bf16(ah[mt], bl[nt], a0, 0, 0, 0);
+          acc[mt][nt] = a0;
+        }
+    }
+    #pragma unroll
+    for (int mt = 0; mt < 2; mt++)
+      #pragma unroll
+      for (int nt = 0; nt < 2; nt++)
+        #pragma unroll
+        for (int r = 0; r < 4; r++) {
+          int rloc = mt * 16 + (lane >> 4) * 4 + r;
+          int col = wcol + nt * 16 + (lane & 15);
+          float g = 2.0f * acc[mt][nt][r] - stValU(sA, rloc, col);
+          storeDual(T20, (brow + rloc) * 128 + col, g);
         }
   }
 }
@@ -925,69 +933,32 @@
   if (tid == 0) scal[72 + b] = red[0] + red[1] + red[2] + red[3];
 }
 
-__global__ __launch_bounds__(256) void k_zfb(float* __restrict__ ws) {
-  __shared__ unsigned short sL[32768];
+__global__ __launch_bounds__(256) void k_b(float* __restrict__ ws) {
+  __shared__ unsigned short sA[8192];
   const unsigned short* Z = MS(ws, sZ);
   const unsigned short* Fm = MS(ws, sF);
   unsigned short* Bbf = (unsigned short*)(ws + fBBF);
   float aeff = ws[fSCAL + 7];
   int tid = threadIdx.x, b = blockIdx.x;
   int w = tid >> 6, lane = tid & 63;
-  int wcol = w * 32, brow = b * 32;
+  int brow = b * 32, wcol = w * 32;
   {
-    f32x4 acc[8][2] = {};
+    f32x4 acc[2][2] = {};
+    #pragma unroll
     for (int ks = 0; ks < 4; ks++) {
       int kb = ks * 32 + (lane >> 4) * 8;
-      short8 bh[2], bl[2];
+      short8 ah[2], al[2], bh[2], bl[2];
+      #pragma unroll
+      for (int mt = 0; mt < 2; mt++) {
+        int r = brow + mt * 16 + (lane & 15);
+        ah[mt] = *(const short8*)(Z + r * 128 + kb);
+        al[mt] = *(const short8*)(Z + 16384 + r * 128 + kb);
+      }
       #pragma unroll
       for (int nt = 0; nt < 2; nt++) {
         int c = wcol + nt * 16 + (lane & 15);
         bh[nt] = *(const short8*)(Fm + c * 128 + kb);
         bl[nt] = *(const short8*)(Fm + 16384 + c * 128 + kb);
-      }
-      #pragma unroll
-      for (int mt = 0; mt < 8; mt++) {
-        int r = mt * 16 + (lane & 15);
-        short8 ah = *(const short8*)(Z + r * 128 + kb);
-        short8 al = *(const short8*)(Z + 16384 + r * 128 + kb);
-        #pragma unroll
-        for (int nt = 0; nt < 2; nt++) {
-          f32x4 a0 = acc[mt][nt];
-          a0 = __builtin_amdgcn_mfma_f32_16x16x32_bf16(ah, bh[nt], a0, 0, 0, 0);
-          a0 = __builtin_amdgcn_mfma_f32_16x16x32_bf16(al, bh[nt], a0, 0, 0, 0);
-          a0 = __builtin_amdgcn_mfma_f32_16x16x32_bf16(ah, bl[nt], a0, 0, 0, 0);
-          acc[mt][nt] = a0;
-        }
-      }
-    }
-    #pragma unroll
-    for (int mt = 0; mt < 8; mt++)
-      #pragma unroll
-      for (int nt = 0; nt < 2; nt++)
-        #pragma unroll
-        for (int r = 0; r < 4; r++) {
-          int row = mt * 16 + (lane >> 4) * 4 + r;
-          int col = wcol + nt * 16 + (lane & 15);
-          ldsPutDual(sL, row, col, acc[mt][nt][r]);
-        }
-  }
-  __syncthreads();
-  {
-    f32x4 acc[2][2] = {};
-    for (int ks = 0; ks < 4; ks++) {
-      int kb = ks * 32 + (lane >> 4) * 8;
-      short8 ah[2], al[2], bh[2], bl[2];
-      #pragma unroll
-      for (int mt = 0; mt < 2; mt++) {
-        int r = brow + mt * 16 + (lane & 15);
-        ah[mt] = lds8(sL, r, kb);
-        al[mt] = lds8(sL + 16384, r, kb);
-      }
-      #pragma unroll
-      for (int nt = 0; nt < 2; nt++) {
-        int c = wcol + nt * 16 + (lane & 15);
-        bh[nt] = *(const short8*)(Z + c * 128 + kb);
-        bl[nt] = *(const short8*)(Z + 16384 + c * 128 + kb);
       }
       #pragma unroll
       for (int mt = 0; mt < 2; mt++)
@@ -1006,9 +977,50 @@
       for (int nt = 0; nt < 2; nt++)
         #pragma unroll
         for (int r = 0; r < 4; r++) {
-          int row = brow + mt * 16 + (lane >> 4) * 4 + r;
+          int rloc = mt * 16 + (lane >> 4) * 4 + r;
           int col = wcol + nt * 16 + (lane & 15);
-          Bbf[row * 128 + col] = f2bf(acc[mt][nt][r] * aeff);
+          stPutDual(sA, rloc, col, acc[mt][nt][r]);
+        }
+  }
+  __syncthreads();
+  {
+    f32x4 acc[2][2] = {};
+    #pragma unroll
+    for (int ks = 0; ks < 4; ks++) {
+      int kb = ks * 32 + (lane >> 4) * 8;
+      short8 ah[2], al[2], bh[2], bl[2];
+      #pragma unroll
+      for (int mt = 0; mt < 2; mt++) {
+        int rloc = mt * 16 + (lane & 15);
+        ah[mt] = st8(sA, rloc, kb);
+        al[mt] = st8(sA + 4096, rloc, kb);
+      }
+      #pragma unroll
+      for (int nt = 0; nt < 2; nt++) {
+        int c = wcol + nt * 16 + (lane & 15);
+        bh[nt] = *(const short8*)(Z + c * 128 + kb);
+        bl[nt] = *(const short8*)(Z + 16384 + c * 128 + kb);
+      }
+      #pragma unroll
+      for (int mt = 0; mt < 2; mt++)
+        #pragma unroll
+        for (int nt = 0; nt < 2; nt++) {
+          f32x4 a0 = acc[mt][nt];
+          a0 = __builtin_amdgcn_mfma_f32_16x16x32_bf16(ah[mt], bh[nt], a0, 0, 0, 0);
+          a0 = __builtin_amdgcn_mfma_f32_16x16x32_bf16(al[mt], bh[nt], a0, 0, 0, 0);
+          a0 = __builtin_amdgcn_mfma_f32_16x16x32_bf16(ah[mt], bl[nt], a0, 0, 0, 0);
+          acc[mt][nt] = a0;
+        }
+    }
+    #pragma unroll
+    for (int mt = 0; mt < 2; mt++)
+      #pragma unroll
+      for (int nt = 0; nt < 2; nt++)
+        #pragma unroll
+        for (int r = 0; r < 4; r++) {
+          int rloc = mt * 16 + (lane >> 4) * 4 + r;
+          int col = wcol + nt * 16 + (lane & 15);
+          Bbf[(brow + rloc) * 128 + col] = f2bf(acc[mt][nt][r] * aeff);
         }
   }
 }
@@ -1151,16 +1163,16 @@
   k_gt_partial<<<64, 256, 0, stream>>>(X, ws);
   k_reduce<<<64, 256, 0, stream>>>(ws);
   k_sbp<<<4, 256, 0, stream>>>(ws);
-  k_p234<<<4, 256, 0, stream>>>(ws);
+  k_pows<<<4, 256, 0, stream>>>(ws);
   k_z<<<4, 256, 0, stream>>>(ws);
-  k_msb<<<4, 256, 0, stream>>>(ws);
-  k_c24<<<4, 256, 0, stream>>>(ws);
+  k_m<<<4, 256, 0, stream>>>(ws);
+  k_c2<<<4, 256, 0, stream>>>(ws);
   k_xh_t2<<<16, 256, 0, stream>>>(ws);
   k_t34<<<8, 256, 0, stream>>>(ws);
   k_t5g<<<20, 256, 0, stream>>>(ws);
-  k_t101520<<<4, 256, 0, stream>>>(ws);
+  k_thi<<<4, 256, 0, stream>>>(ws);
   k_bigF<<<4, 256, 0, stream>>>(ws);
-  k_zfb<<<4, 256, 0, stream>>>(ws);
+  k_b<<<4, 256, 0, stream>>>(ws);
   k_latent<<<64, 256, 0, stream>>>(test, ws);
   k_pair<<<dim3(64, 64), 256, 0, stream>>>(ws, out);
 }
```

New measurement: 265.4 us. -11.7%, faster.
